# Kernel tuning notes

Measured on AMD Instinct MI355X. Metric: run time of the kernel, lower is better.

## Reference

```python
import jax, jax.numpy as jnp
import numpy as np

N_NODES = 25000
N_EDGES = 400000
FEAT = 128
HID = 64
HEADS = 4
NUM_CLASSES = 2
NUM_GRAPHS = 64


def setup_inputs() -> dict:
    key = jax.random.key(0)
    ks = jax.random.split(key, 16)
    x = jax.random.normal(ks[0], (N_NODES, FEAT), dtype=jnp.float32)
    edge_index = jax.random.randint(ks[1], (2, N_EDGES), 0, N_NODES, dtype=jnp.int32)
    batch = jnp.sort(jax.random.randint(ks[2], (N_NODES,), 0, NUM_GRAPHS, dtype=jnp.int32))
    s = 1.0 / np.sqrt(FEAT)
    sh = 1.0 / np.sqrt(HID)
    shc = 1.0 / np.sqrt(HID * HEADS)
    return {
        "x": x,
        "edge_index": edge_index,
        "batch": batch,
        # conv1: GraphConv(FEAT -> HID): lin_rel (bias) on aggregated neighbors + lin_root (no bias)
        "W1_rel": jax.random.uniform(ks[3], (FEAT, HID), jnp.float32, -s, s),
        "b1": jnp.zeros((HID,), jnp.float32),
        "W1_root": jax.random.uniform(ks[4], (FEAT, HID), jnp.float32, -s, s),
        # conv3: GATConv(HID -> HID, heads=HEADS), concat output [N, HEADS*HID]
        "Wg": jax.random.uniform(ks[5], (HID, HEADS * HID), jnp.float32, -sh, sh),
        "att_src": jax.random.uniform(ks[6], (HEADS, HID), jnp.float32, -sh, sh),
        "att_dst": jax.random.uniform(ks[7], (HEADS, HID), jnp.float32, -sh, sh),
        "bg": jnp.zeros((HEADS * HID,), jnp.float32),
        # conv5: GraphConv(HEADS*HID -> HID)
        "W5_rel": jax.random.uniform(ks[8], (HEADS * HID, HID), jnp.float32, -shc, shc),
        "b5": jnp.zeros((HID,), jnp.float32),
        "W5_root": jax.random.uniform(ks[9], (HEADS * HID, HID), jnp.float32, -shc, shc),
        # fc head
        "W_fc1": jax.random.uniform(ks[10], (HID, HID), jnp.float32, -sh, sh),
        "b_fc1": jnp.zeros((HID,), jnp.float32),
        "W_fc2": jax.random.uniform(ks[11], (HID, NUM_CLASSES), jnp.float32, -sh, sh),
        "b_fc2": jnp.zeros((NUM_CLASSES,), jnp.float32),
    }


def _graph_conv(h, src, dst, W_rel, b, W_root):
    # PyG GraphConv (aggr='add'): out_i = W_rel @ sum_{j->i} h_j + b + W_root @ h_i
    agg = jax.ops.segment_sum(h[src], dst, num_segments=N_NODES)
    return agg @ W_rel + b + h @ W_root


def _gat_conv(h, src, dst, Wg, att_src, att_dst, bg):
    # GATConv with default add_self_loops=True; eval mode (no attn dropout)
    n = h.shape[0]
    loop = jnp.arange(n, dtype=src.dtype)
    si = jnp.concatenate([src, loop])
    di = jnp.concatenate([dst, loop])
    xl = (h @ Wg).reshape(n, HEADS, HID)              # [N, H, C]
    a_s = jnp.sum(xl * att_src, axis=-1)              # [N, H]
    a_d = jnp.sum(xl * att_dst, axis=-1)              # [N, H]
    e = jax.nn.leaky_relu(a_s[si] + a_d[di], 0.2)     # [E', H]
    m = jax.ops.segment_max(e, di, num_segments=n)
    p = jnp.exp(e - m[di])
    denom = jax.ops.segment_sum(p, di, num_segments=n)
    alpha = p / denom[di]                             # segment softmax over incoming edges
    out = jax.ops.segment_sum(alpha[:, :, None] * xl[si], di, num_segments=n)
    return out.reshape(n, HEADS * HID) + bg


def reference(x, edge_index, batch, W1_rel, b1, W1_root, Wg, att_src, att_dst, bg,
              W5_rel, b5, W5_root, W_fc1, b_fc1, W_fc2, b_fc2):
    src, dst = edge_index[0], edge_index[1]
    h = jax.nn.relu(_graph_conv(x, src, dst, W1_rel, b1, W1_root))
    h = jax.nn.relu(_gat_conv(h, src, dst, Wg, att_src, att_dst, bg))
    h = jax.nn.relu(_graph_conv(h, src, dst, W5_rel, b5, W5_root))
    g = jax.ops.segment_sum(h, batch, num_segments=NUM_GRAPHS)   # global_add_pool
    g = jax.nn.relu(g @ W_fc1 + b_fc1)
    return jax.nn.sigmoid(g @ W_fc2 + b_fc2)
```

## Files before the change

kernel.cpp:

```cpp
#include <hip/hip_runtime.h>
#include <math.h>

#define N_NODES 25000
#define N_EDGES 400000
#define FEAT 128
#define HID 64
#define HEADS 4
#define HH 256
#define NUM_GRAPHS 64
#define BUCKET 96
#define HS 1601536
#define NPH 25600
#define FILL_BLOCKS 1563

typedef unsigned short ushort_t;
typedef unsigned int uint_t;
typedef __attribute__((ext_vector_type(8))) short short8;
typedef __attribute__((ext_vector_type(4))) float f32x4;

__device__ __forceinline__ float lrelu(float x){ return x > 0.f ? x : 0.2f*x; }

__device__ __forceinline__ ushort_t f2bf(float f){
  uint_t u = __float_as_uint(f);
  return (ushort_t)((u + 0x7fffu + ((u >> 16) & 1u)) >> 16);
}
#define BF_LO(u) __uint_as_float((u) << 16)
#define BF_HI(u) __uint_as_float((u) & 0xffff0000u)

__global__ __launch_bounds__(256) void k_init(
    const float* __restrict__ W1_rel, const float* __restrict__ W1_root,
    const float* __restrict__ W5_rel, const float* __restrict__ W5_root,
    const float* __restrict__ Wg,
    ushort_t* __restrict__ wc1b, ushort_t* __restrict__ wc5b,
    ushort_t* __restrict__ wgb, float* __restrict__ g )
{
  const int e = blockIdx.x*256 + threadIdx.x;
  {
    int j=e&7, lane=(e>>3)&63, kc=(e>>9)&3, nt=e>>11;
    int k = kc*32 + (lane>>4)*8 + j, n = nt*16 + (lane&15);
    float v = (n < 64) ? W1_rel[k*64 + n] : W1_root[k*64 + n - 64];
    wc1b[e] = f2bf(v);
  }
  {
    int j=e&7, lane=(e>>3)&63, kt=(e>>9)&1, nt=e>>10;
    int k = kt*32 + (lane>>4)*8 + j, n = nt*16 + (lane&15);
    wgb[e] = f2bf(Wg[k*HH + n]);
  }
  #pragma unroll
  for (int e5 = e; e5 < 32768; e5 += 16384){
    int j=e5&7, lane=(e5>>3)&63, kc=(e5>>9)&7, nt=e5>>12;
    int k = kc*32 + (lane>>4)*8 + j, n = nt*16 + (lane&15);
    float v = (n < 64) ? W5_rel[k*64 + n] : W5_root[k*64 + n - 64];
    wc5b[e5] = f2bf(v);
  }
  int* z = (int*)g;
  for (int i = e; i < 4096 + N_NODES; i += 16384) z[i] = 0;
}

__global__ __launch_bounds__(256) void k_c1_fill(
    const int* __restrict__ src, const int* __restrict__ dst,
    int* __restrict__ cnt, int* __restrict__ slot,
    const float* __restrict__ X, const ushort_t* __restrict__ wc1b,
    const float* __restrict__ bias,
    ushort_t* __restrict__ out_rel_b, float* __restrict__ out_root)
{
  if (blockIdx.x < FILL_BLOCKS){
    const int e = blockIdx.x*256 + threadIdx.x;
    if (e < N_EDGES){
      int d = dst[e];
      int pos = atomicAdd(&cnt[d], 1);
      if (pos < BUCKET) slot[(size_t)d*BUCKET + pos] = src[e];
    }
    return;
  }
  const int wid  = __builtin_amdgcn_readfirstlane(threadIdx.x >> 6);
  const int lane = threadIdx.x & 63;
  const int quad = lane >> 4, col = lane & 15;
  const int nb = (blockIdx.x - FILL_BLOCKS)*64 + wid*16;
  if (nb >= N_NODES) return;
  const int row = min(nb + col, N_NODES-1);
  const float* __restrict__ xr = X + (size_t)row*FEAT + quad*8;
  short8 a[4];
  #pragma unroll
  for (int kc = 0; kc < 4; kc++){
    #pragma unroll
    for (int j = 0; j < 8; j++)
      ((ushort_t*)&a[kc])[j] = f2bf(xr[kc*32 + j]);
  }
  #pragma unroll
  for (int nt = 0; nt < 8; nt++){
    f32x4 d = {0.f,0.f,0.f,0.f};
    #pragma unroll
    for (int kc = 0; kc < 4; kc++){
      short8 b = *(const short8*)(wc1b + ((size_t)(nt*4+kc)*64 + lane)*8);
      d = __builtin_amdgcn_mfma_f32_16x16x32_bf16(a[kc], b, d, 0, 0, 0);
    }
    if (nt < 4){
      #pragma unroll
      for (int r = 0; r < 4; r++){
        const int node = nb + quad*4 + r;
        if (node < N_NODES)
          out_rel_b[(size_t)node*HID + nt*16 + col] = f2bf(d[r]);
      }
    } else {
      const float bv = bias[(nt-4)*16 + col];
      #pragma unroll
      for (int r = 0; r < 4; r++){
        const int node = nb + quad*4 + r;
        if (node < N_NODES)
          out_root[(size_t)node*HID + (nt-4)*16 + col] = d[r] + bv;
      }
    }
  }
}

__global__ __launch_bounds__(256) void conv5_mfma(
    const ushort_t* __restrict__ h2b_hm, const ushort_t* __restrict__ wc5b,
    const float* __restrict__ bias,
    ushort_t* __restrict__ out_rel_b, float* __restrict__ out_root)
{
  const int wid  = __builtin_amdgcn_readfirstlane(threadIdx.x >> 6);
  const int lane = threadIdx.x & 63;
  const int quad = lane >> 4, col = lane & 15;
  const int nb = blockIdx.x*64 + wid*16;
  if (nb >= N_NODES) return;
  const int row = nb + col;
  short8 a[8];
  #pragma unroll
  for (int kc = 0; kc < 8; kc++){
    const int k0 = kc*32 + quad*8;
    a[kc] = *(const short8*)(h2b_hm + (size_t)(k0>>6)*HS
                             + (size_t)row*HID + (k0&63));
  }
  #pragma unroll
  for (int nt = 0; nt < 8; nt++){
    f32x4 d = {0.f,0.f,0.f,0.f};
    #pragma unroll
    for (int kc = 0; kc < 8; kc++){
      short8 b = *(const short8*)(wc5b + ((size_t)(nt*8+kc)*64 + lane)*8);
      d = __builtin_amdgcn_mfma_f32_16x16x32_bf16(a[kc], b, d, 0, 0, 0);
    }
    if (nt < 4){
      #pragma unroll
      for (int r = 0; r < 4; r++){
        const int node = nb + quad*4 + r;
        if (node < N_NODES)
          out_rel_b[(size_t)node*HID + nt*16 + col] = f2bf(d[r]);
      }
    } else {
      const float bv = bias[(nt-4)*16 + col];
      #pragma unroll
      for (int r = 0; r < 4; r++){
        const int node = nb + quad*4 + r;
        if (node < N_NODES)
          out_root[(size_t)node*HID + (nt-4)*16 + col] = d[r] + bv;
      }
    }
  }
}

__global__ __launch_bounds__(256) void k3_mfma(
    const ushort_t* __restrict__ h1b, const ushort_t* __restrict__ wgb,
    const float* __restrict__ att_src, const float* __restrict__ att_dst,
    ushort_t* __restrict__ xlb_hm, float* __restrict__ a_s_hm,
    float* __restrict__ a_d_hm)
{
  const int wid  = __builtin_amdgcn_readfirstlane(threadIdx.x >> 6);
  const int lane = threadIdx.x & 63;
  const int quad = lane >> 4, col = lane & 15;
  const int nb = blockIdx.x*64 + wid*16;
  const ushort_t* arow = h1b + (size_t)(nb + col)*HID + quad*8;
  short8 a0 = *(const short8*)(arow);
  short8 a1 = *(const short8*)(arow + 32);
  float as_acc[4] = {0,0,0,0}, ad_acc[4] = {0,0,0,0};
  #pragma unroll
  for (int nt = 0; nt < 16; nt++){
    short8 b0 = *(const short8*)(wgb + ((size_t)(nt*2+0)*64 + lane)*8);
    short8 b1 = *(const short8*)(wgb + ((size_t)(nt*2+1)*64 + lane)*8);
    f32x4 d = {0.f, 0.f, 0.f, 0.f};
    d = __builtin_amdgcn_mfma_f32_16x16x32_bf16(a0, b0, d, 0, 0, 0);
    d = __builtin_amdgcn_mfma_f32_16x16x32_bf16(a1, b1, d, 0, 0, 0);
    const int h = nt >> 2;
    const float asv = att_src[h*HID + (nt & 3)*16 + col];
    const float adv = att_dst[h*HID + (nt & 3)*16 + col];
    #pragma unroll
    for (int r = 0; r < 4; r++){
      const int node = nb + quad*4 + r;
      if (node < N_NODES)
        xlb_hm[(size_t)h*HS + (size_t)node*HID + (nt&3)*16 + col] = f2bf(d[r]);
      as_acc[r] += d[r]*asv;
      ad_acc[r] += d[r]*adv;
    }
    if ((nt & 3) == 3){
      #pragma unroll
      for (int r = 0; r < 4; r++){
        float s1 = as_acc[r], s2 = ad_acc[r];
        #pragma unroll
        for (int off = 1; off < 16; off <<= 1){
          s1 += __shfl_xor(s1, off, 64);
          s2 += __shfl_xor(s2, off, 64);
        }
        const int node = nb + quad*4 + r;
        if (col == 0 && node < N_NODES){
          a_s_hm[h*NPH + node] = s1;
          a_d_hm[h*NPH + node] = s2;
        }
        as_acc[r] = 0.f; ad_acc[r] = 0.f;
      }
    }
  }
}

template<int MODE>
__global__ __launch_bounds__(256) void k_aggb(
    const int* __restrict__ cnt, const int* __restrict__ slot,
    const ushort_t* __restrict__ featb, const float* __restrict__ root,
    const int* __restrict__ batch, float* __restrict__ g,
    ushort_t* __restrict__ outb)
{
  const int node = blockIdx.x*4 + (threadIdx.x >> 6);
  const int lane = threadIdx.x & 63;
  const int* __restrict__ sl = slot + (size_t)node*BUCKET;
  const int deg = min(cnt[node], BUCKET);
  float acc = root[(size_t)node*HID + lane];
  int e = 0;
  for (; e + 4 <= deg; e += 4){
    int sA = sl[e],   sB = sl[e+1];
    int sC = sl[e+2], sD = sl[e+3];
    acc += BF_LO((uint_t)featb[(size_t)sA*HID + lane]);
    acc += BF_LO((uint_t)featb[(size_t)sB*HID + lane]);
    acc += BF_LO((uint_t)featb[(size_t)sC*HID + lane]);
    acc += BF_LO((uint_t)featb[(size_t)sD*HID + lane]);
  }
  for (; e < deg; e++)
    acc += BF_LO((uint_t)featb[(size_t)sl[e]*HID + lane]);
  const float v = fmaxf(acc, 0.f);
  if (MODE == 0){
    outb[(size_t)node*HID + lane] = f2bf(v);
  } else {
    const int b = batch[node];
    atomicAdd(&g[b*HID + lane], v);
  }
}

__global__ __launch_bounds__(256) void k_gat_node(
    const int* __restrict__ cnt, const int* __restrict__ slot,
    const ushort_t* __restrict__ xlb_hm, const float* __restrict__ a_s_hm,
    const float* __restrict__ a_d_hm, const float* __restrict__ bg,
    ushort_t* __restrict__ h2b_hm)
{
  const int head = blockIdx.x & 3;
  const int node = (blockIdx.x >> 2)*16 + (threadIdx.x >> 4);
  if (node >= N_NODES) return;
  const int lane = threadIdx.x & 63;
  const int cl = lane & 15;
  const int gb = lane & 48;
  const int* __restrict__ sl = slot + (size_t)node*BUCKET;
  const int deg = min(cnt[node], BUCKET);
  const ushort_t* __restrict__ xlh = xlb_hm + (size_t)head*HS;
  const float* __restrict__ ash = a_s_hm + head*NPH;
  const float adh = a_d_hm[head*NPH + node];
  float acc0=0, acc1=0, acc2=0, acc3=0;
  float dsum = 0.f;
  for (int base = 0; base < deg; base += 16){
    float pme = 0.f; int sme = node;
    const int e = base + cl;
    if (e < deg){
      sme = sl[e];
      pme = __expf(lrelu(ash[sme] + adh));
    }
    dsum += pme;
    const int nsub = min(16, deg - base);
    int s = 0;
    for (; s + 2 <= nsub; s += 2){
      const float pA = __shfl(pme, gb + s, 64);
      const int   sA = __shfl(sme, gb + s, 64);
      const float pB = __shfl(pme, gb + s + 1, 64);
      const int   sB = __shfl(sme, gb + s + 1, 64);
      uint2 rA = ((const uint2*)(xlh + (size_t)sA*HID))[cl];
      uint2 rB = ((const uint2*)(xlh + (size_t)sB*HID))[cl];
      acc0 += pA*BF_LO(rA.x); acc1 += pA*BF_HI(rA.x);
      acc2 += pA*BF_LO(rA.y); acc3 += pA*BF_HI(rA.y);
      acc0 += pB*BF_LO(rB.x); acc1 += pB*BF_HI(rB.x);
      acc2 += pB*BF_LO(rB.y); acc3 += pB*BF_HI(rB.y);
    }
    if (s < nsub){
      const float pA = __shfl(pme, gb + s, 64);
      const int   sA = __shfl(sme, gb + s, 64);
      uint2 rA = ((const uint2*)(xlh + (size_t)sA*HID))[cl];
      acc0 += pA*BF_LO(rA.x); acc1 += pA*BF_HI(rA.x);
      acc2 += pA*BF_LO(rA.y); acc3 += pA*BF_HI(rA.y);
    }
  }
  #pragma unroll
  for (int off = 1; off < 16; off <<= 1) dsum += __shfl_xor(dsum, off, 64);
  const float pself = __expf(lrelu(ash[node] + adh));
  const float inv = 1.f / (dsum + pself);
  uint2 r = ((const uint2*)(xlh + (size_t)node*HID))[cl];
  acc0 += pself*BF_LO(r.x); acc1 += pself*BF_HI(r.x);
  acc2 += pself*BF_LO(r.y); acc3 += pself*BF_HI(r.y);
  const int col0 = head*HID + cl*4;
  const float ox = fmaxf(acc0*inv + bg[col0+0], 0.f);
  const float oy = fmaxf(acc1*inv + bg[col0+1], 0.f);
  const float oz = fmaxf(acc2*inv + bg[col0+2], 0.f);
  const float ow = fmaxf(acc3*inv + bg[col0+3], 0.f);
  uint2 o;
  o.x = (uint_t)f2bf(ox) | ((uint_t)f2bf(oy) << 16);
  o.y = (uint_t)f2bf(oz) | ((uint_t)f2bf(ow) << 16);
  ((uint2*)(h2b_hm + (size_t)head*HS + (size_t)node*HID))[cl] = o;
}

__global__ __launch_bounds__(256) void k_head(
    const float* __restrict__ g, const float* __restrict__ W1,
    const float* __restrict__ b1, const float* __restrict__ W2,
    const float* __restrict__ b2, float* __restrict__ out)
{
  __shared__ float gs[NUM_GRAPHS*HID];
  __shared__ float hh[NUM_GRAPHS*HID];
  for (int i = threadIdx.x; i < NUM_GRAPHS*HID; i += 256) gs[i] = g[i];
  __syncthreads();
  for (int t = threadIdx.x; t < NUM_GRAPHS*HID; t += 256){
    int b = t >> 6, j = t & 63;
    float acc = b1[j];
    for (int k = 0; k < HID; k++) acc += gs[b*HID+k]*W1[k*HID+j];
    hh[t] = fmaxf(acc, 0.f);
  }
  __syncthreads();
  for (int t = threadIdx.x; t < NUM_GRAPHS*2; t += 256){
    int b = t >> 1, c = t & 1;
    float acc = b2[c];
    for (int k = 0; k < HID; k++) acc += hh[b*HID+k]*W2[k*2+c];
    out[t] = 1.f / (1.f + __expf(-acc));
  }
}

extern "C" void kernel_launch(void* const* d_in, const int* in_sizes, int n_in,
                              void* d_out, int out_size, void* d_ws, size_t ws_size,
                              hipStream_t stream)
{
  const float* x       = (const float*)d_in[0];
  const int*   ei      = (const int*)d_in[1];
  const int*   batch   = (const int*)d_in[2];
  const float* W1_rel  = (const float*)d_in[3];
  const float* b1      = (const float*)d_in[4];
  const float* W1_root = (const float*)d_in[5];
  const float* Wg      = (const float*)d_in[6];
  const float* att_src = (const float*)d_in[7];
  const float* att_dst = (const float*)d_in[8];
  const float* bg      = (const float*)d_in[9];
  const float* W5_rel  = (const float*)d_in[10];
  const float* b5      = (const float*)d_in[11];
  const float* W5_root = (const float*)d_in[12];
  const float* W_fc1   = (const float*)d_in[13];
  const float* b_fc1   = (const float*)d_in[14];
  const float* W_fc2   = (const float*)d_in[15];
  const float* b_fc2   = (const float*)d_in[16];
  const int* src = ei;
  const int* dst = ei + N_EDGES;

  float* ws    = (float*)d_ws;
  ushort_t* xr_b   = (ushort_t*)ws;
  float*    hB     = ws +  800800;
  ushort_t* h1b    = (ushort_t*)(ws + 2402400);
  ushort_t* xlb_hm = (ushort_t*)(ws + 3203200);
  float*    a_s_hm = ws + 6406304;
  float*    a_d_hm = ws + 6508704;
  ushort_t* h2b_hm = (ushort_t*)(ws + 6611104);
  float*    g      = ws + 9814200;
  int*      cnt    = (int*)(ws + 9818296);
  ushort_t* wc1b   = (ushort_t*)(ws + 9843296);
  ushort_t* wc5b   = (ushort_t*)(ws + 9851488);
  ushort_t* wgb    = (ushort_t*)(ws + 9867872);
  int*      slot   = (int*)(ws + 9876064);
  float*    out    = (float*)d_out;
  (void)cnt;

  k_init<<<64,256,0,stream>>>(W1_rel, W1_root, W5_rel, W5_root, Wg,
                              wc1b, wc5b, wgb, g);

  k_c1_fill<<<FILL_BLOCKS + (N_NODES+63)/64,256,0,stream>>>(
      src, dst, (int*)(ws + 9818296), (int*)(ws + 9876064),
      x, wc1b, b1, xr_b, hB);

  k_aggb<0><<<N_NODES/4,256,0,stream>>>((int*)(ws + 9818296), (int*)(ws + 9876064),
      xr_b, hB, nullptr, nullptr, h1b);

  k3_mfma<<<(N_NODES+63)/64,256,0,stream>>>(h1b, wgb, att_src, att_dst,
                                            xlb_hm, a_s_hm, a_d_hm);
  k_gat_node<<<((N_NODES+15)/16)*HEADS,256,0,stream>>>((int*)(ws + 9818296),
      (int*)(ws + 9876064), xlb_hm, a_s_hm, a_d_hm, bg, h2b_hm);

  conv5_mfma<<<(N_NODES+63)/64,256,0,stream>>>(h2b_hm, wc5b, b5, xr_b, hB);
  k_aggb<1><<<N_NODES/4,256,0,stream>>>((int*)(ws + 9818296), (int*)(ws + 9876064),
      xr_b, hB, batch, g, nullptr);

  k_head<<<1,256,0,stream>>>(g, W_fc1, b_fc1, W_fc2, b_fc2, out);
}
```

Measured before the change: 253.5 us.

## Compress edge slots to 16-bit, root to bf16, batch neighbor gathers

Edge slot indices are stored as 16-bit values and the root term as bf16, halving their memory traffic in the fill, aggregation and GAT kernels. The aggregation kernel loads the first 32 slot indices with four vector loads and issues up to 32 independent feature gathers before summing, to expose more memory-level parallelism. Node ids up to 25000 fit in 16 bits, but the root term loses precision, and the unrolled 32-entry register array raises register pressure.

```diff
diff --git a/kernel.cpp b/kernel.cpp
--- a/kernel.cpp
+++ b/kernel.cpp
@@ -59,17 +59,17 @@
 
 __global__ __launch_bounds__(256) void k_c1_fill(
     const int* __restrict__ src, const int* __restrict__ dst,
-    int* __restrict__ cnt, int* __restrict__ slot,
+    int* __restrict__ cnt, ushort_t* __restrict__ slot,
     const float* __restrict__ X, const ushort_t* __restrict__ wc1b,
     const float* __restrict__ bias,
-    ushort_t* __restrict__ out_rel_b, float* __restrict__ out_root)
+    ushort_t* __restrict__ out_rel_b, ushort_t* __restrict__ out_root_b)
 {
   if (blockIdx.x < FILL_BLOCKS){
     const int e = blockIdx.x*256 + threadIdx.x;
     if (e < N_EDGES){
       int d = dst[e];
       int pos = atomicAdd(&cnt[d], 1);
-      if (pos < BUCKET) slot[(size_t)d*BUCKET + pos] = src[e];
+      if (pos < BUCKET) slot[(size_t)d*BUCKET + pos] = (ushort_t)src[e];
     }
     return;
   }
@@ -108,7 +108,7 @@
       for (int r = 0; r < 4; r++){
         const int node = nb + quad*4 + r;
         if (node < N_NODES)
-          out_root[(size_t)node*HID + (nt-4)*16 + col] = d[r] + bv;
+          out_root_b[(size_t)node*HID + (nt-4)*16 + col] = f2bf(d[r] + bv);
       }
     }
   }
@@ -117,7 +117,7 @@
 __global__ __launch_bounds__(256) void conv5_mfma(
     const ushort_t* __restrict__ h2b_hm, const ushort_t* __restrict__ wc5b,
     const float* __restrict__ bias,
-    ushort_t* __restrict__ out_rel_b, float* __restrict__ out_root)
+    ushort_t* __restrict__ out_rel_b, ushort_t* __restrict__ out_root_b)
 {
   const int wid  = __builtin_amdgcn_readfirstlane(threadIdx.x >> 6);
   const int lane = threadIdx.x & 63;
@@ -153,7 +153,7 @@
       for (int r = 0; r < 4; r++){
         const int node = nb + quad*4 + r;
         if (node < N_NODES)
-          out_root[(size_t)node*HID + (nt-4)*16 + col] = d[r] + bv;
+          out_root_b[(size_t)node*HID + (nt-4)*16 + col] = f2bf(d[r] + bv);
       }
     }
   }
@@ -213,27 +213,38 @@
 
 template<int MODE>
 __global__ __launch_bounds__(256) void k_aggb(
-    const int* __restrict__ cnt, const int* __restrict__ slot,
-    const ushort_t* __restrict__ featb, const float* __restrict__ root,
+    const int* __restrict__ cnt, const ushort_t* __restrict__ slot,
+    const ushort_t* __restrict__ featb, const ushort_t* __restrict__ rootb,
     const int* __restrict__ batch, float* __restrict__ g,
     ushort_t* __restrict__ outb)
 {
   const int node = blockIdx.x*4 + (threadIdx.x >> 6);
   const int lane = threadIdx.x & 63;
-  const int* __restrict__ sl = slot + (size_t)node*BUCKET;
+  const ushort_t* __restrict__ sl = slot + (size_t)node*BUCKET;
   const int deg = min(cnt[node], BUCKET);
-  float acc = root[(size_t)node*HID + lane];
-  int e = 0;
-  for (; e + 4 <= deg; e += 4){
-    int sA = sl[e],   sB = sl[e+1];
-    int sC = sl[e+2], sD = sl[e+3];
-    acc += BF_LO((uint_t)featb[(size_t)sA*HID + lane]);
-    acc += BF_LO((uint_t)featb[(size_t)sB*HID + lane]);
-    acc += BF_LO((uint_t)featb[(size_t)sC*HID + lane]);
-    acc += BF_LO((uint_t)featb[(size_t)sD*HID + lane]);
-  }
-  for (; e < deg; e++)
-    acc += BF_LO((uint_t)featb[(size_t)sl[e]*HID + lane]);
+  const int4 A = ((const int4*)sl)[0];
+  const int4 B = ((const int4*)sl)[1];
+  const int4 C = ((const int4*)sl)[2];
+  const int4 D = ((const int4*)sl)[3];
+  const int w[16] = {A.x,A.y,A.z,A.w, B.x,B.y,B.z,B.w,
+                     C.x,C.y,C.z,C.w, D.x,D.y,D.z,D.w};
+  uint_t uu[32];
+  #pragma unroll
+  for (int k = 0; k < 32; k++) uu[k] = 0u;
+  #pragma unroll
+  for (int k = 0; k < 32; k++){
+    if (deg > k){
+      const int s = (k & 1) ? ((w[k>>1] >> 16) & 0xffff) : (w[k>>1] & 0xffff);
+      uu[k] = featb[(size_t)s*HID + lane];
+    }
+  }
+  float acc = BF_LO((uint_t)rootb[(size_t)node*HID + lane]);
+  #pragma unroll
+  for (int k = 0; k < 32; k++) acc += BF_LO(uu[k]);
+  for (int t = 32; t < deg; t++){
+    const int s = sl[t];
+    acc += BF_LO((uint_t)featb[(size_t)s*HID + lane]);
+  }
   const float v = fmaxf(acc, 0.f);
   if (MODE == 0){
     outb[(size_t)node*HID + lane] = f2bf(v);
@@ -244,7 +255,7 @@
 }
 
 __global__ __launch_bounds__(256) void k_gat_node(
-    const int* __restrict__ cnt, const int* __restrict__ slot,
+    const int* __restrict__ cnt, const ushort_t* __restrict__ slot,
     const ushort_t* __restrict__ xlb_hm, const float* __restrict__ a_s_hm,
     const float* __restrict__ a_d_hm, const float* __restrict__ bg,
     ushort_t* __restrict__ h2b_hm)
@@ -255,7 +266,7 @@
   const int lane = threadIdx.x & 63;
   const int cl = lane & 15;
   const int gb = lane & 48;
-  const int* __restrict__ sl = slot + (size_t)node*BUCKET;
+  const ushort_t* __restrict__ sl = slot + (size_t)node*BUCKET;
   const int deg = min(cnt[node], BUCKET);
   const ushort_t* __restrict__ xlh = xlb_hm + (size_t)head*HS;
   const float* __restrict__ ash = a_s_hm + head*NPH;
@@ -360,7 +371,7 @@
 
   float* ws    = (float*)d_ws;
   ushort_t* xr_b   = (ushort_t*)ws;
-  float*    hB     = ws +  800800;
+  ushort_t* rootb  = (ushort_t*)(ws + 800800);
   ushort_t* h1b    = (ushort_t*)(ws + 2402400);
   ushort_t* xlb_hm = (ushort_t*)(ws + 3203200);
   float*    a_s_hm = ws + 6406304;
@@ -371,28 +382,24 @@
   ushort_t* wc1b   = (ushort_t*)(ws + 9843296);
   ushort_t* wc5b   = (ushort_t*)(ws + 9851488);
   ushort_t* wgb    = (ushort_t*)(ws + 9867872);
-  int*      slot   = (int*)(ws + 9876064);
+  ushort_t* slot   = (ushort_t*)(ws + 9876064);
   float*    out    = (float*)d_out;
-  (void)cnt;
 
   k_init<<<64,256,0,stream>>>(W1_rel, W1_root, W5_rel, W5_root, Wg,
                               wc1b, wc5b, wgb, g);
 
   k_c1_fill<<<FILL_BLOCKS + (N_NODES+63)/64,256,0,stream>>>(
-      src, dst, (int*)(ws + 9818296), (int*)(ws + 9876064),
-      x, wc1b, b1, xr_b, hB);
-
-  k_aggb<0><<<N_NODES/4,256,0,stream>>>((int*)(ws + 9818296), (int*)(ws + 9876064),
-      xr_b, hB, nullptr, nullptr, h1b);
+      src, dst, cnt, slot, x, wc1b, b1, xr_b, rootb);
+
+  k_aggb<0><<<N_NODES/4,256,0,stream>>>(cnt, slot, xr_b, rootb, nullptr, nullptr, h1b);
 
   k3_mfma<<<(N_NODES+63)/64,256,0,stream>>>(h1b, wgb, att_src, att_dst,
                                             xlb_hm, a_s_hm, a_d_hm);
-  k_gat_node<<<((N_NODES+15)/16)*HEADS,256,0,stream>>>((int*)(ws + 9818296),
-      (int*)(ws + 9876064), xlb_hm, a_s_hm, a_d_hm, bg, h2b_hm);
-
-  conv5_mfma<<<(N_NODES+63)/64,256,0,stream>>>(h2b_hm, wc5b, b5, xr_b, hB);
-  k_aggb<1><<<N_NODES/4,256,0,stream>>>((int*)(ws + 9818296), (int*)(ws + 9876064),
-      xr_b, hB, batch, g, nullptr);
+  k_gat_node<<<((N_NODES+15)/16)*HEADS,256,0,stream>>>(cnt, slot,
+      xlb_hm, a_s_hm, a_d_hm, bg, h2b_hm);
+
+  conv5_mfma<<<(N_NODES+63)/64,256,0,stream>>>(h2b_hm, wc5b, b5, xr_b, rootb);
+  k_aggb<1><<<N_NODES/4,256,0,stream>>>(cnt, slot, xr_b, rootb, batch, g, nullptr);
 
   k_head<<<1,256,0,stream>>>(g, W_fc1, b_fc1, W_fc2, b_fc2, out);
 }
```

After: 276.4 us. 1.09x slower.
